# Performance work log

Hardware: AMD Instinct MI355X
Metric: run time of the kernel (lower is better)

Reference implementation:

```python
import jax, jax.numpy as jnp
import numpy as np

# graph/batch constants
B, N_PER, DEG, FEAT, K = 64, 1024, 16, 64, 10
N = B * N_PER            # 65536 total nodes
E = N * DEG              # 1048576 edges
HID = 2 * FEAT           # 128


def setup_inputs() -> dict:
    key = jax.random.key(0)
    ks = jax.random.split(key, 10)
    x = jax.random.normal(ks[0], (N, FEAT), jnp.float32)
    # intra-graph edges: local indices in [0, n) offset by graph id * n
    offs = (jnp.arange(B, dtype=jnp.int32) * N_PER)[:, None]
    edge_src = (jax.random.randint(ks[1], (B, N_PER * DEG), 0, N_PER, jnp.int32) + offs).reshape(-1)
    edge_dst = (jax.random.randint(ks[2], (B, N_PER * DEG), 0, N_PER, jnp.int32) + offs).reshape(-1)
    uniforms = jax.random.uniform(ks[3], (N, 3 * K), jnp.float32, 1e-6, 1.0 - 1e-6)

    def lin(k, i, o):
        s = 1.0 / np.sqrt(i)
        return jax.random.uniform(k, (i, o), jnp.float32, -s, s)

    return {
        "x": x, "edge_src": edge_src, "edge_dst": edge_dst, "uniforms": uniforms,
        "W0": lin(ks[4], FEAT, HID), "b0": jnp.zeros((HID,), jnp.float32),
        "W1": lin(ks[5], HID, HID), "b1": jnp.zeros((HID,), jnp.float32),
        "Wf": lin(ks[6], HID, HID), "bf": jnp.zeros((HID,), jnp.float32),
        "W2": lin(ks[7], 2 * HID, HID), "b2": jnp.zeros((HID,), jnp.float32),
        "W3": lin(ks[8], HID, 1), "b3": jnp.zeros((1,), jnp.float32),
    }


def _gcn_norm(src, dst):
    # GCNConv: add self-loops, symmetric deg^{-1/2} normalization
    loop = jnp.arange(N, dtype=src.dtype)
    s = jnp.concatenate([src, loop])
    d = jnp.concatenate([dst, loop])
    deg = jnp.zeros((N,), jnp.float32).at[d].add(1.0)
    dinv = jax.lax.rsqrt(deg)  # deg >= 1 because of self-loops
    return s, d, dinv[s] * dinv[d]


def _gcn(h, W, b, s, d, norm):
    h = h @ W                                                   # [N, out]
    agg = jnp.zeros((N, W.shape[1]), h.dtype).at[d].add(h[s] * norm[:, None])
    return agg + b


def reference(x, edge_src, edge_dst, uniforms, W0, b0, W1, b1, Wf, bf, W2, b2, W3, b3):
    s, d, norm = _gcn_norm(edge_src, edge_dst)
    # conv0 + global max pool + fc1 -> per-graph global info
    h0 = jax.nn.relu(_gcn(x, W0, b0, s, d, norm))               # [N, HID]
    glob = jnp.max(h0.reshape(B, N_PER, HID), axis=1) @ Wf + bf  # [B, HID]
    # two applications of the SAME conv1 (as in the source)
    h = jax.nn.relu(_gcn(h0, W1, b1, s, d, norm))
    h = jax.nn.relu(_gcn(h, W1, b1, s, d, norm))
    # ConcatenateLayer: [local, tiled global] per node (dropout is eval identity)
    h = jnp.concatenate([h, jnp.repeat(glob, N_PER, axis=0)], axis=-1)  # [N, 2*HID]
    h = jax.nn.relu(_gcn(h, W2, b2, s, d, norm))
    logits = _gcn(h, W3, b3, s, d, norm).reshape(B, N_PER)      # [B, n]
    # SampleConcrete (eval): per-graph top-k threshold mask
    th = jax.lax.top_k(logits, K)[0][:, -1]                     # kth-largest per graph
    mask = (logits >= th[:, None]).astype(jnp.float32)
    return mask.reshape(N, 1)
```

## Files before the change

kernel.cpp:

```cpp
#include <hip/hip_runtime.h>
#include <math.h>

#define NB    64
#define NPER  1024
#define NTOT  65536
#define ETOT  1048576
#define FEAT  64
#define HID   128
#define KSEL  10
#define MAXDEG 64


typedef __attribute__((ext_vector_type(8))) short bf16x8;
typedef __attribute__((ext_vector_type(4))) float f32x4;

static __device__ __forceinline__ unsigned short f2bf(float x) {
    unsigned u = __float_as_uint(x);
    return (unsigned short)((u + 0x7FFFu + ((u >> 16) & 1u)) >> 16);
}
static __device__ __forceinline__ float bf2f(unsigned short s) {
    return __uint_as_float(((unsigned)s) << 16);
}

__global__ __launch_bounds__(256) void csr_k(const int* __restrict__ src,
                                             const int* __restrict__ dst,
                                             int* __restrict__ cnt,
                                             unsigned short* __restrict__ col16) {
    int e = blockIdx.x * 256 + threadIdx.x;
    if (e >= ETOT) return;
    int d = dst[e];
    int s = src[e];
    int pos = atomicAdd(&cnt[d], 1);
    col16[(size_t)pos * NTOT + d] = (unsigned short)(s & (NPER - 1));
}

__global__ __launch_bounds__(256) void pack_k(const float* __restrict__ W0,
                                              const float* __restrict__ W1,
                                              const float* __restrict__ W2,
                                              unsigned short* __restrict__ Wph,
                                              unsigned short* __restrict__ Wpl) {
    int t = blockIdx.x * 256 + threadIdx.x;
    if (t >= 320 * 128) return;
    int k = t >> 7;
    int c = t & 127;
    float v;
    size_t mb;
    int kk;
    if (k < 64)       { kk = k;       v = W0[kk * 128 + c]; mb = 0; }
    else if (k < 192) { kk = k - 64;  v = W1[kk * 128 + c]; mb = (size_t)64 * 128; }
    else              { kk = k - 192; v = W2[kk * 128 + c]; mb = (size_t)192 * 128; }
    unsigned short h  = f2bf(v);
    unsigned short lo = f2bf(v - bf2f(h));
    size_t d = mb + ((size_t)(kk >> 3) * 128 + c) * 8 + (kk & 7);
    Wph[d] = h;
    Wpl[d] = lo;
}

__global__ __launch_bounds__(1024) void agg_k(const float* __restrict__ Z,
                                              const float* __restrict__ x,
                                              const unsigned short* __restrict__ col16,
                                              const int* __restrict__ cnt,
                                              unsigned short* __restrict__ Ah,
                                              unsigned short* __restrict__ Al,
                                              int cshift,
                                              float* __restrict__ fvec) {
    __shared__ float4 sy4[4096];
    int t = threadIdx.x;
    int g = blockIdx.x >> cshift;
    int c = blockIdx.x & ((1 << cshift) - 1);
    int gbase = g << 10;

    if (x) {
#pragma unroll
        for (int j = 0; j < 4; ++j) {
            int fl = j * 1024 + t;
            int v = fl >> 2, q = fl & 3;
            float dvv = rsqrtf((float)cnt[gbase + v] + 1.0f);
            float4 z = *(const float4*)&x[(size_t)(gbase + v) * FEAT + c * 16 + q * 4];
            z.x *= dvv; z.y *= dvv; z.z *= dvv; z.w *= dvv;
            sy4[fl] = z;
        }
    } else {
        const float4* Zg4 = (const float4*)(Z + ((size_t)c * NTOT + gbase) * 16);
#pragma unroll
        for (int j = 0; j < 4; ++j) sy4[j * 1024 + t] = Zg4[j * 1024 + t];
    }
    __syncthreads();

    int f4 = t & 3;
    int vl = t >> 2;

#pragma unroll 1
    for (int pass = 0; pass < 4; ++pass) {
        int v = pass * 256 + vl;
        int gv = gbase + v;
        int n = cnt[gv];
        float dv = rsqrtf((float)n + 1.0f);
        const unsigned short* ip = col16 + gv;
        float4 acc = sy4[v * 4 + f4];
        int i = 0;
        for (; i + 2 <= n; i += 2) {
            int a = ip[(size_t)i * NTOT];
            int b = ip[(size_t)(i + 1) * NTOT];
            float4 ya = sy4[a * 4 + f4];
            float4 yb = sy4[b * 4 + f4];
            acc.x += ya.x + yb.x;
            acc.y += ya.y + yb.y;
            acc.z += ya.z + yb.z;
            acc.w += ya.w + yb.w;
        }
        if (i < n) {
            float4 ya = sy4[(int)ip[(size_t)i * NTOT] * 4 + f4];
            acc.x += ya.x; acc.y += ya.y; acc.z += ya.z; acc.w += ya.w;
        }
        acc.x *= dv; acc.y *= dv; acc.z *= dv; acc.w *= dv;
        int krow = c * 16 + f4 * 4;
        size_t ba = ((size_t)(krow >> 3) * NTOT + gv) * 8 + (krow & 7);
        ushort4 h, lo;
        h.x = f2bf(acc.x); lo.x = f2bf(acc.x - bf2f(h.x));
        h.y = f2bf(acc.y); lo.y = f2bf(acc.y - bf2f(h.y));
        h.z = f2bf(acc.z); lo.z = f2bf(acc.z - bf2f(h.z));
        h.w = f2bf(acc.w); lo.w = f2bf(acc.w - bf2f(h.w));
        *(ushort4*)&Ah[ba] = h;
        *(ushort4*)&Al[ba] = lo;
    }

    if (fvec && c == 0) {
        __syncthreads();
        float* sdv = (float*)sy4;
        float dv = rsqrtf((float)cnt[gbase + t] + 1.0f);
        sdv[t] = dv;
        __syncthreads();
        int n = cnt[gbase + t];
        float acc = dv;
        const unsigned short* ip = col16 + gbase + t;
        for (int i = 0; i < n; ++i) acc += sdv[ip[(size_t)i * NTOT]];
        fvec[gbase + t] = dv * acc;
    }
}

__global__ __launch_bounds__(256, 4) void gemm_k(const unsigned short* __restrict__ Ah,
                                                 const unsigned short* __restrict__ Al,
                                                 const unsigned short* __restrict__ Wph,
                                                 const unsigned short* __restrict__ Wpl,
                                                 const float* __restrict__ bias,
                                                 float* __restrict__ outZ,
                                                 int K,
                                                 const float* __restrict__ fvec,
                                                 const float* __restrict__ gproj,
                                                 float* __restrict__ part,
                                                 const float* __restrict__ W3,
                                                 const int* __restrict__ cnt,
                                                 float* __restrict__ zout) {
    __shared__ __align__(16) unsigned short sAh[4 * 64 * 8];
    __shared__ __align__(16) unsigned short sAl[4 * 64 * 8];
    __shared__ __align__(16) unsigned short sWh[4 * 128 * 8];
    __shared__ __align__(16) unsigned short sWl[4 * 128 * 8];
    __shared__ float zred[4 * 64];

    int t = threadIdx.x;
    int row0 = blockIdx.x * 64;
    int w = t >> 6;
    int l = t & 63;
    int lr = l & 15;
    int hg = l >> 4;

    f32x4 acc[4][2];
#pragma unroll
    for (int m = 0; m < 4; ++m)
#pragma unroll
        for (int n = 0; n < 2; ++n) acc[m][n] = (f32x4){0.f, 0.f, 0.f, 0.f};

    int nk = K >> 5;
#pragma unroll 1
    for (int s = 0; s < nk; ++s) {
        {
            int gg = t >> 6, row = t & 63;
            size_t src = ((size_t)(s * 4 + gg) * NTOT + row0 + row) * 8;
            *(uint4*)&sAh[t * 8] = *(const uint4*)&Ah[src];
            *(uint4*)&sAl[t * 8] = *(const uint4*)&Al[src];
        }
        {
            size_t base = (size_t)s * 4096;
            *(uint4*)&sWh[t * 8]         = *(const uint4*)&Wph[base + t * 8];
            *(uint4*)&sWh[(t + 256) * 8] = *(const uint4*)&Wph[base + (t + 256) * 8];
            *(uint4*)&sWl[t * 8]         = *(const uint4*)&Wpl[base + t * 8];
            *(uint4*)&sWl[(t + 256) * 8] = *(const uint4*)&Wpl[base + (t + 256) * 8];
        }
        __syncthreads();
        bf16x8 ah[4], al[4], bh[2], bl[2];
#pragma unroll
        for (int m = 0; m < 4; ++m) {
            ah[m] = *(const bf16x8*)&sAh[(hg * 64 + m * 16 + lr) * 8];
            al[m] = *(const bf16x8*)&sAl[(hg * 64 + m * 16 + lr) * 8];
        }
#pragma unroll
        for (int n = 0; n < 2; ++n) {
            bh[n] = *(const bf16x8*)&sWh[(hg * 128 + w * 32 + n * 16 + lr) * 8];
            bl[n] = *(const bf16x8*)&sWl[(hg * 128 + w * 32 + n * 16 + lr) * 8];
        }
#pragma unroll
        for (int m = 0; m < 4; ++m)
#pragma unroll
            for (int n = 0; n < 2; ++n) {
                acc[m][n] = __builtin_amdgcn_mfma_f32_16x16x32_bf16(ah[m], bh[n], acc[m][n], 0, 0, 0);
                acc[m][n] = __builtin_amdgcn_mfma_f32_16x16x32_bf16(al[m], bh[n], acc[m][n], 0, 0, 0);
                acc[m][n] = __builtin_amdgcn_mfma_f32_16x16x32_bf16(ah[m], bl[n], acc[m][n], 0, 0, 0);
            }
        __syncthreads();
    }

    int g = row0 >> 10;
    int wc0 = w * 32;
    float bb[2], gp[2], w3c[2];
#pragma unroll
    for (int n = 0; n < 2; ++n) {
        int col = wc0 + n * 16 + lr;
        bb[n]  = bias[col];
        gp[n]  = fvec ? gproj[(size_t)g * 128 + col] : 0.f;
        w3c[n] = zout ? W3[col] : 0.f;
    }
    float fr[4][4];
    if (fvec) {
#pragma unroll
        for (int m = 0; m < 4; ++m)
#pragma unroll
            for (int r = 0; r < 4; ++r) fr[m][r] = fvec[row0 + m * 16 + hg * 4 + r];
    }
    float dvs[4][4];
    if (outZ) {
#pragma unroll
        for (int m = 0; m < 4; ++m)
#pragma unroll
            for (int r = 0; r < 4; ++r)
                dvs[m][r] = rsqrtf((float)cnt[row0 + m * 16 + hg * 4 + r] + 1.0f);
    }
    float zp[4][4];
#pragma unroll
    for (int m = 0; m < 4; ++m)
#pragma unroll
        for (int r = 0; r < 4; ++r) zp[m][r] = 0.f;
    float cmx[2] = {0.f, 0.f};

#pragma unroll
    for (int m = 0; m < 4; ++m)
#pragma unroll
        for (int n = 0; n < 2; ++n)
#pragma unroll
            for (int r = 0; r < 4; ++r) {
                float v = acc[m][n][r] + bb[n];
                if (fvec) v += fr[m][r] * gp[n];
                v = fmaxf(v, 0.f);
                if (part) cmx[n] = fmaxf(cmx[n], v);
                if (zout) zp[m][r] += v * w3c[n];
                if (outZ) {
                    int row = row0 + m * 16 + hg * 4 + r;
                    int cidx = w * 2 + n;
                    outZ[((size_t)cidx * NTOT + row) * 16 + lr] = v * dvs[m][r];
                }
            }

    if (part) {
#pragma unroll
        for (int n = 0; n < 2; ++n) {
            float v = cmx[n];
            v = fmaxf(v, __shfl_xor(v, 16));
            v = fmaxf(v, __shfl_xor(v, 32));
            if (hg == 0)
                atomicMax((int*)&part[(size_t)g * 128 + wc0 + n * 16 + lr],
                          __float_as_int(v));
        }
    }

    if (zout) {
#pragma unroll
        for (int m = 0; m < 4; ++m)
#pragma unroll
            for (int r = 0; r < 4; ++r) {
                float v = zp[m][r];
                v += __shfl_xor(v, 1);
                v += __shfl_xor(v, 2);
                v += __shfl_xor(v, 4);
                v += __shfl_xor(v, 8);
                zp[m][r] = v;
            }
        if (lr == 0) {
#pragma unroll
            for (int m = 0; m < 4; ++m)
#pragma unroll
                for (int r = 0; r < 4; ++r)
                    zred[w * 64 + m * 16 + hg * 4 + r] = zp[m][r];
        }
        __syncthreads();
        if (t < 64) {
            float sZ = zred[t] + zred[64 + t] + zred[128 + t] + zred[192 + t];
            zout[row0 + t] = sZ * rsqrtf((float)cnt[row0 + t] + 1.0f);
        }
    }
}

__global__ __launch_bounds__(128) void glob_k(const float* __restrict__ part,
                                              const float* __restrict__ Wf,
                                              const float* __restrict__ bf,
                                              const float* __restrict__ W2,
                                              float* __restrict__ gproj) {
    __shared__ float mp[128];
    __shared__ float gl[128];
    int g = blockIdx.x, t = threadIdx.x;
    mp[t] = part[(size_t)g * 128 + t];
    __syncthreads();
    float acc = bf[t];
    for (int k = 0; k < 128; ++k) acc += mp[k] * Wf[(size_t)k * 128 + t];
    gl[t] = acc;
    __syncthreads();
    float acc2 = 0.f;
    for (int k = 0; k < 128; ++k) acc2 += gl[k] * W2[(size_t)(128 + k) * 128 + t];
    gproj[(size_t)g * 128 + t] = acc2;
}

__global__ __launch_bounds__(256) void smask_k(const float* __restrict__ z,
                                               const unsigned short* __restrict__ col16,
                                               const int* __restrict__ cnt,
                                               const float* __restrict__ b3,
                                               float* __restrict__ out) {
    __shared__ float sz[1024];
    __shared__ float sl[1024];
    __shared__ float slo[1024];
    __shared__ float rv[256];
    __shared__ int   ri[256];
    __shared__ float sth;
    int g = blockIdx.x, t = threadIdx.x;
    int base = g << 10;
#pragma unroll
    for (int i = 0; i < 4; ++i) sz[t + 256 * i] = z[base + t + 256 * i];
    __syncthreads();
    float bb = b3[0];
#pragma unroll 1
    for (int i = 0; i < 4; ++i) {
        int v = t + 256 * i;
        int gv = base + v;
        int n = cnt[gv];
        float dv = rsqrtf((float)n + 1.0f);
        float acc = sz[v];
        const unsigned short* ip = col16 + gv;
        int j = 0;
        for (; j + 2 <= n; j += 2)
            acc += sz[ip[(size_t)j * NTOT]] + sz[ip[(size_t)(j + 1) * NTOT]];
        for (; j < n; ++j) acc += sz[ip[(size_t)j * NTOT]];
        float lg = acc * dv + bb;
        sl[v] = lg; slo[v] = lg;
    }
    __syncthreads();
    for (int pass = 0; pass < KSEL; ++pass) {
        float bv = -INFINITY;
        int bi = 0;
#pragma unroll
        for (int i = 0; i < 4; ++i) {
            float v = sl[t + 256 * i];
            if (v > bv) { bv = v; bi = t + 256 * i; }
        }
        rv[t] = bv; ri[t] = bi;
        __syncthreads();
        for (int s = 128; s > 0; s >>= 1) {
            if (t < s) {
                if (rv[t + s] > rv[t]) { rv[t] = rv[t + s]; ri[t] = ri[t + s]; }
            }
            __syncthreads();
        }
        if (t == 0) { sth = rv[0]; sl[ri[0]] = -INFINITY; }
        __syncthreads();
    }
    float th = sth;
#pragma unroll
    for (int i = 0; i < 4; ++i) {
        int v = t + 256 * i;
        out[base + v] = (slo[v] >= th) ? 1.f : 0.f;
    }
}

extern "C" void kernel_launch(void* const* d_in, const int* in_sizes, int n_in,
                              void* d_out, int out_size, void* d_ws, size_t ws_size,
                              hipStream_t stream) {
    const float* x        = (const float*)d_in[0];
    const int*   edge_src = (const int*)d_in[1];
    const int*   edge_dst = (const int*)d_in[2];
    const float* W0 = (const float*)d_in[4];
    const float* b0 = (const float*)d_in[5];
    const float* W1 = (const float*)d_in[6];
    const float* b1 = (const float*)d_in[7];
    const float* Wf = (const float*)d_in[8];
    const float* bf = (const float*)d_in[9];
    const float* W2 = (const float*)d_in[10];
    const float* b2 = (const float*)d_in[11];
    const float* W3 = (const float*)d_in[12];
    const float* b3 = (const float*)d_in[13];
    float* out = (float*)d_out;

    char* w = (char*)d_ws;
    int*            cnt   = (int*)w;            w += (size_t)NTOT * 4;
    unsigned short* col16 = (unsigned short*)w; w += (size_t)NTOT * MAXDEG * 2;
    float*          fvec  = (float*)w;          w += (size_t)NTOT * 4;
    unsigned short* Ah    = (unsigned short*)w; w += (size_t)NTOT * 128 * 2;
    unsigned short* Al    = (unsigned short*)w; w += (size_t)NTOT * 128 * 2;
    float*          Q     = (float*)w;          w += (size_t)NTOT * 128 * 4;
    float*          part  = (float*)w;          w += (size_t)NB * 128 * 4;
    float*          gproj = (float*)w;          w += (size_t)NB * 128 * 4;
    float*          z     = (float*)w;          w += (size_t)NTOT * 4;
    unsigned short* Wph   = (unsigned short*)w; w += (size_t)320 * 128 * 2;
    unsigned short* Wpl   = (unsigned short*)w; w += (size_t)320 * 128 * 2;

    hipMemsetAsync(cnt, 0, (size_t)NTOT * 4, stream);
    hipMemsetAsync(part, 0, (size_t)NB * 128 * 4, stream);
    csr_k<<<ETOT / 256, 256, 0, stream>>>(edge_src, edge_dst, cnt, col16);
    pack_k<<<160, 256, 0, stream>>>(W0, W1, W2, Wph, Wpl);

    agg_k<<<NB * 4, 1024, 0, stream>>>(nullptr, x, col16, cnt, Ah, Al, 2, nullptr);
    gemm_k<<<NTOT / 64, 256, 0, stream>>>(Ah, Al, Wph, Wpl, b0, Q, FEAT,
                                          nullptr, nullptr, part, nullptr, cnt, nullptr);

    glob_k<<<NB, 128, 0, stream>>>(part, Wf, bf, W2, gproj);

    agg_k<<<NB * 8, 1024, 0, stream>>>(Q, nullptr, col16, cnt, Ah, Al, 3, nullptr);
    gemm_k<<<NTOT / 64, 256, 0, stream>>>(Ah, Al, Wph + 64 * 128, Wpl + 64 * 128, b1, Q,
                                          HID, nullptr, nullptr, nullptr, nullptr, cnt,
                                          nullptr);
    agg_k<<<NB * 8, 1024, 0, stream>>>(Q, nullptr, col16, cnt, Ah, Al, 3, nullptr);
    gemm_k<<<NTOT / 64, 256, 0, stream>>>(Ah, Al, Wph + 64 * 128, Wpl + 64 * 128, b1, Q,
                                          HID, nullptr, nullptr, nullptr, nullptr, cnt,
                                          nullptr);

    agg_k<<<NB * 8, 1024, 0, stream>>>(Q, nullptr, col16, cnt, Ah, Al, 3, fvec);
    gemm_k<<<NTOT / 64, 256, 0, stream>>>(Ah, Al, Wph + 192 * 128, Wpl + 192 * 128, b2,
                                          nullptr, HID, fvec, gproj, nullptr, W3, cnt, z);

    smask_k<<<NB, 256, 0, stream>>>(z, col16, cnt, b3, out);
}
```

Baseline: 323.4 us.

## Preload full A tile in GEMM, read weights from global, unroll gather, warp-shuffle top-k

The GEMM kernel now loads the whole 64-row A tile (all K) into shared memory once and reads the packed weights directly from global/L2 instead of staging them per k-step, which removes the per-step barriers. Its launch-bounds occupancy hint drops from 4 to 3 to fit the larger shared buffers. The aggregation gather loop is unrolled by 4 for more memory-level parallelism. The top-k argmax reduction uses wave shuffles instead of a shared-memory tree, and the memset of the partial buffer is folded into the pack kernel. The risks are lower occupancy and uncached, uncoalesced-looking weight reads from global memory.

```diff
diff --git a/kernel.cpp b/kernel.cpp
--- a/kernel.cpp
+++ b/kernel.cpp
@@ -38,7 +38,11 @@
                                               const float* __restrict__ W1,
                                               const float* __restrict__ W2,
                                               unsigned short* __restrict__ Wph,
-                                              unsigned short* __restrict__ Wpl) {
+                                              unsigned short* __restrict__ Wpl,
+                                              float* __restrict__ part) {
+    if (blockIdx.x == 0) {
+        for (int i = threadIdx.x; i < NB * 128; i += 256) part[i] = 0.f;
+    }
     int t = blockIdx.x * 256 + threadIdx.x;
     if (t >= 320 * 128) return;
     int k = t >> 7;
@@ -99,17 +103,21 @@
         const unsigned short* ip = col16 + gv;
         float4 acc = sy4[v * 4 + f4];
         int i = 0;
-        for (; i + 2 <= n; i += 2) {
-            int a = ip[(size_t)i * NTOT];
-            int b = ip[(size_t)(i + 1) * NTOT];
-            float4 ya = sy4[a * 4 + f4];
-            float4 yb = sy4[b * 4 + f4];
-            acc.x += ya.x + yb.x;
-            acc.y += ya.y + yb.y;
-            acc.z += ya.z + yb.z;
-            acc.w += ya.w + yb.w;
-        }
-        if (i < n) {
+        for (; i + 4 <= n; i += 4) {
+            int a0 = ip[(size_t)(i + 0) * NTOT];
+            int a1 = ip[(size_t)(i + 1) * NTOT];
+            int a2 = ip[(size_t)(i + 2) * NTOT];
+            int a3 = ip[(size_t)(i + 3) * NTOT];
+            float4 y0 = sy4[a0 * 4 + f4];
+            float4 y1 = sy4[a1 * 4 + f4];
+            float4 y2 = sy4[a2 * 4 + f4];
+            float4 y3 = sy4[a3 * 4 + f4];
+            acc.x += (y0.x + y1.x) + (y2.x + y3.x);
+            acc.y += (y0.y + y1.y) + (y2.y + y3.y);
+            acc.z += (y0.z + y1.z) + (y2.z + y3.z);
+            acc.w += (y0.w + y1.w) + (y2.w + y3.w);
+        }
+        for (; i < n; ++i) {
             float4 ya = sy4[(int)ip[(size_t)i * NTOT] * 4 + f4];
             acc.x += ya.x; acc.y += ya.y; acc.z += ya.z; acc.w += ya.w;
         }
@@ -139,7 +147,7 @@
     }
 }
 
-__global__ __launch_bounds__(256, 4) void gemm_k(const unsigned short* __restrict__ Ah,
+__global__ __launch_bounds__(256, 3) void gemm_k(const unsigned short* __restrict__ Ah,
                                                  const unsigned short* __restrict__ Al,
                                                  const unsigned short* __restrict__ Wph,
                                                  const unsigned short* __restrict__ Wpl,
@@ -152,10 +160,8 @@
                                                  const float* __restrict__ W3,
                                                  const int* __restrict__ cnt,
                                                  float* __restrict__ zout) {
-    __shared__ __align__(16) unsigned short sAh[4 * 64 * 8];
-    __shared__ __align__(16) unsigned short sAl[4 * 64 * 8];
-    __shared__ __align__(16) unsigned short sWh[4 * 128 * 8];
-    __shared__ __align__(16) unsigned short sWl[4 * 128 * 8];
+    __shared__ __align__(16) unsigned short sAh[64 * 128];
+    __shared__ __align__(16) unsigned short sAl[64 * 128];
     __shared__ float zred[4 * 64];
 
     int t = threadIdx.x;
@@ -171,33 +177,31 @@
 #pragma unroll
         for (int n = 0; n < 2; ++n) acc[m][n] = (f32x4){0.f, 0.f, 0.f, 0.f};
 
+    int nu = (K >> 3) << 6 >> 8;
+    for (int i = 0; i < nu; ++i) {
+        int u = t + i * 256;
+        int p = u >> 6, r = u & 63;
+        size_t src = ((size_t)p * NTOT + row0 + r) * 8;
+        *(uint4*)&sAh[u * 8] = *(const uint4*)&Ah[src];
+        *(uint4*)&sAl[u * 8] = *(const uint4*)&Al[src];
+    }
+    __syncthreads();
+
     int nk = K >> 5;
 #pragma unroll 1
     for (int s = 0; s < nk; ++s) {
-        {
-            int gg = t >> 6, row = t & 63;
-            size_t src = ((size_t)(s * 4 + gg) * NTOT + row0 + row) * 8;
-            *(uint4*)&sAh[t * 8] = *(const uint4*)&Ah[src];
-            *(uint4*)&sAl[t * 8] = *(const uint4*)&Al[src];
-        }
-        {
-            size_t base = (size_t)s * 4096;
-            *(uint4*)&sWh[t * 8]         = *(const uint4*)&Wph[base + t * 8];
-            *(uint4*)&sWh[(t + 256) * 8] = *(const uint4*)&Wph[base + (t + 256) * 8];
-            *(uint4*)&sWl[t * 8]         = *(const uint4*)&Wpl[base + t * 8];
-            *(uint4*)&sWl[(t + 256) * 8] = *(const uint4*)&Wpl[base + (t + 256) * 8];
-        }
-        __syncthreads();
+        int pb = s * 4 + hg;
         bf16x8 ah[4], al[4], bh[2], bl[2];
 #pragma unroll
         for (int m = 0; m < 4; ++m) {
-            ah[m] = *(const bf16x8*)&sAh[(hg * 64 + m * 16 + lr) * 8];
-            al[m] = *(const bf16x8*)&sAl[(hg * 64 + m * 16 + lr) * 8];
+            ah[m] = *(const bf16x8*)&sAh[(pb * 64 + m * 16 + lr) * 8];
+            al[m] = *(const bf16x8*)&sAl[(pb * 64 + m * 16 + lr) * 8];
         }
 #pragma unroll
         for (int n = 0; n < 2; ++n) {
-            bh[n] = *(const bf16x8*)&sWh[(hg * 128 + w * 32 + n * 16 + lr) * 8];
-            bl[n] = *(const bf16x8*)&sWl[(hg * 128 + w * 32 + n * 16 + lr) * 8];
+            size_t wb = ((size_t)pb * 128 + w * 32 + n * 16 + lr) * 8;
+            bh[n] = *(const bf16x8*)&Wph[wb];
+            bl[n] = *(const bf16x8*)&Wpl[wb];
         }
 #pragma unroll
         for (int m = 0; m < 4; ++m)
@@ -207,7 +211,6 @@
                 acc[m][n] = __builtin_amdgcn_mfma_f32_16x16x32_bf16(al[m], bh[n], acc[m][n], 0, 0, 0);
                 acc[m][n] = __builtin_amdgcn_mfma_f32_16x16x32_bf16(ah[m], bl[n], acc[m][n], 0, 0, 0);
             }
-        __syncthreads();
     }
 
     int g = row0 >> 10;
@@ -326,10 +329,11 @@
     __shared__ float sz[1024];
     __shared__ float sl[1024];
     __shared__ float slo[1024];
-    __shared__ float rv[256];
-    __shared__ int   ri[256];
+    __shared__ float rv[4];
+    __shared__ int   ri[4];
     __shared__ float sth;
     int g = blockIdx.x, t = threadIdx.x;
+    int wv = t >> 6, ln = t & 63;
     int base = g << 10;
 #pragma unroll
     for (int i = 0; i < 4; ++i) sz[t + 256 * i] = z[base + t + 256 * i];
@@ -359,15 +363,21 @@
             float v = sl[t + 256 * i];
             if (v > bv) { bv = v; bi = t + 256 * i; }
         }
-        rv[t] = bv; ri[t] = bi;
+#pragma unroll
+        for (int off = 32; off; off >>= 1) {
+            float ov = __shfl_xor(bv, off);
+            int   oi = __shfl_xor(bi, off);
+            if (ov > bv || (ov == bv && oi < bi)) { bv = ov; bi = oi; }
+        }
+        if (ln == 0) { rv[wv] = bv; ri[wv] = bi; }
         __syncthreads();
-        for (int s = 128; s > 0; s >>= 1) {
-            if (t < s) {
-                if (rv[t + s] > rv[t]) { rv[t] = rv[t + s]; ri[t] = ri[t + s]; }
-            }
-            __syncthreads();
-        }
-        if (t == 0) { sth = rv[0]; sl[ri[0]] = -INFINITY; }
+        if (t == 0) {
+            float mv = rv[0]; int mi = ri[0];
+#pragma unroll
+            for (int q = 1; q < 4; ++q)
+                if (rv[q] > mv || (rv[q] == mv && ri[q] < mi)) { mv = rv[q]; mi = ri[q]; }
+            sth = mv; sl[mi] = -INFINITY;
+        }
         __syncthreads();
     }
     float th = sth;
@@ -410,9 +420,8 @@
     unsigned short* Wpl   = (unsigned short*)w; w += (size_t)320 * 128 * 2;
 
     hipMemsetAsync(cnt, 0, (size_t)NTOT * 4, stream);
-    hipMemsetAsync(part, 0, (size_t)NB * 128 * 4, stream);
     csr_k<<<ETOT / 256, 256, 0, stream>>>(edge_src, edge_dst, cnt, col16);
-    pack_k<<<160, 256, 0, stream>>>(W0, W1, W2, Wph, Wpl);
+    pack_k<<<160, 256, 0, stream>>>(W0, W1, W2, Wph, Wpl, part);
 
     agg_k<<<NB * 4, 1024, 0, stream>>>(nullptr, x, col16, cnt, Ah, Al, 2, nullptr);
     gemm_k<<<NTOT / 64, 256, 0, stream>>>(Ah, Al, Wph, Wpl, b0, Q, FEAT,
```

New measurement: 310.2 us. 4.1% less time.
